# Kernel optimization log

Measured on AMD Instinct MI355X. Metric: run time of the kernel, lower is better.

Reference implementation:

```python
import jax, jax.numpy as jnp
import numpy as np

PATCH = 14   # vision_config.patch_size
MERGE = 2    # spatial_merge_size
D = 1024     # vision_config.hidden_size
# pixel (H, W) per image; all dims divisible by PATCH*MERGE = 28
IMAGE_SIZES = np.array([[1540, 1232], [1120, 1540], [896, 1260],
                        [1540, 1540], [1260, 896], [728, 1540]], dtype=np.int64)


def setup_inputs() -> dict:
    key = jax.random.key(0)
    k1, k2 = jax.random.split(key)
    hs = IMAGE_SIZES[:, 0] // PATCH
    ws = IMAGE_SIZES[:, 1] // PATCH
    total_tokens = int(np.sum(hs * ws))  # 47820
    image_features = jax.random.normal(k1, (total_tokens, D), dtype=jnp.float32)
    # nn.Linear(D*MERGE**2 -> D, bias=False): weight [D, D*MERGE**2]
    weight = jax.random.normal(k2, (D, D * MERGE * MERGE), dtype=jnp.float32) * 0.02
    return {"image_features": image_features, "weight": weight,
            "image_sizes": IMAGE_SIZES}


def _merge_patches(image_features, image_sizes):
    """Per-image unfold(kernel=stride=MERGE) -> [n_blocks, D*MERGE^2], concatenated."""
    m = MERGE
    d = image_features.shape[-1]
    sizes = np.asarray(image_sizes)
    hs = sizes[:, 0] // PATCH
    ws = sizes[:, 1] // PATCH
    offsets = np.concatenate([[0], np.cumsum(hs * ws)])
    grids = []
    for i in range(sizes.shape[0]):
        h, w = int(hs[i]), int(ws[i])
        x = jax.lax.dynamic_slice_in_dim(image_features, int(offsets[i]), h * w, 0)
        # [h, w, d] -> blocks of m x m; torch unfold layout is (d, kh, kw) channel-major
        x = x.reshape(h // m, m, w // m, m, d)
        x = x.transpose(0, 2, 4, 1, 3)           # [h/m, w/m, d, m, m]
        x = x.reshape((h // m) * (w // m), d * m * m)
        grids.append(x)
    return jnp.concatenate(grids, axis=0)        # [sum(h*w)/m^2, d*m^2]


def reference(image_features, weight, image_sizes):
    merged = _merge_patches(image_features, image_sizes)
    return merged @ weight.T                     # [N_merged, D]
```

## Files before the change

### kernel.cpp

```cpp
#include <hip/hip_runtime.h>
#include <hip/hip_bf16.h>
#include <stdint.h>

#define K_DIM 4096
#define N_DIM 1024
#define M_TOT 11955

__constant__ int c_wm[6]     = {44, 55, 45, 55, 32, 55};
__constant__ int c_w[6]      = {88, 110, 90, 110, 64, 110};
__constant__ int c_tokoff[6] = {0, 9680, 18480, 24240, 36340, 42100};
__constant__ int c_blkoff[6] = {0, 2420, 4620, 6060, 9085, 10525};

typedef __attribute__((ext_vector_type(8))) short bf16x8;
typedef __attribute__((ext_vector_type(4))) float f32x4;

__global__ __launch_bounds__(256) void merge_cvt(
    const float* __restrict__ feat, __hip_bfloat16* __restrict__ merged)
{
    const int r = blockIdx.x;
    int img = 0;
#pragma unroll
    for (int t = 1; t < 6; ++t)
        if (r >= c_blkoff[t]) img = t;
    const int bi = r - c_blkoff[img];
    const int wm = c_wm[img];
    const int i = bi / wm;
    const int j = bi - i * wm;
    const int w = c_w[img];

    const size_t base00 = ((size_t)c_tokoff[img] + (size_t)(2 * i) * w + 2 * j) * N_DIM;
    const size_t base01 = base00 + N_DIM;
    const size_t base10 = base00 + (size_t)w * N_DIM;
    const size_t base11 = base10 + N_DIM;

    __hip_bfloat16* outrow = merged + (size_t)r * K_DIM;

    for (int c = threadIdx.x; c < K_DIM / 8; c += 256) {
        const int d2 = 2 * c;
        float2 f00 = *(const float2*)(feat + base00 + d2);
        float2 f01 = *(const float2*)(feat + base01 + d2);
        float2 f10 = *(const float2*)(feat + base10 + d2);
        float2 f11 = *(const float2*)(feat + base11 + d2);
        union { __hip_bfloat16 h[8]; uint4 u; } pk;
        pk.h[0] = __float2bfloat16(f00.x);
        pk.h[1] = __float2bfloat16(f01.x);
        pk.h[2] = __float2bfloat16(f10.x);
        pk.h[3] = __float2bfloat16(f11.x);
        pk.h[4] = __float2bfloat16(f00.y);
        pk.h[5] = __float2bfloat16(f01.y);
        pk.h[6] = __float2bfloat16(f10.y);
        pk.h[7] = __float2bfloat16(f11.y);
        *(uint4*)(outrow + 8 * c) = pk.u;
    }
}

__global__ __launch_bounds__(256) void wcvt(
    const float* __restrict__ src, __hip_bfloat16* __restrict__ dst)
{
    const int idx = blockIdx.x * 256 + threadIdx.x;
    const float4* s = (const float4*)src + (size_t)idx * 2;
    float4 a = s[0], b = s[1];
    union { __hip_bfloat16 h[8]; uint4 u; } pk;
    pk.h[0] = __float2bfloat16(a.x);
    pk.h[1] = __float2bfloat16(a.y);
    pk.h[2] = __float2bfloat16(a.z);
    pk.h[3] = __float2bfloat16(a.w);
    pk.h[4] = __float2bfloat16(b.x);
    pk.h[5] = __float2bfloat16(b.y);
    pk.h[6] = __float2bfloat16(b.z);
    pk.h[7] = __float2bfloat16(b.w);
    *((uint4*)dst + idx) = pk.u;
}

#define BM 128
#define BN 128
#define BK 32

__global__ __launch_bounds__(256) void gemm_bt(
    const __hip_bfloat16* __restrict__ A,
    const __hip_bfloat16* __restrict__ B,
    float* __restrict__ C)
{
    __shared__ __align__(16) __hip_bfloat16 lA[BM * BK];
    __shared__ __align__(16) __hip_bfloat16 lB[BN * BK];

    const int tid = threadIdx.x;
    const int lane = tid & 63;
    const int wave = tid >> 6;
    const int m0 = blockIdx.y * BM;
    const int n0 = blockIdx.x * BN;
    const int wm = (wave >> 1) * 64;
    const int wn = (wave & 1) * 64;
    const int al = lane & 15;
    const int q = lane >> 4;

    const int r0 = tid >> 2;
    const int kp = (tid & 3) * 8;

    int ga0 = m0 + r0;       if (ga0 > M_TOT - 1) ga0 = M_TOT - 1;
    int ga1 = m0 + r0 + 64;  if (ga1 > M_TOT - 1) ga1 = M_TOT - 1;
    const __hip_bfloat16* gA0 = A + (size_t)ga0 * K_DIM + kp;
    const __hip_bfloat16* gA1 = A + (size_t)ga1 * K_DIM + kp;
    const __hip_bfloat16* gB0 = B + (size_t)(n0 + r0) * K_DIM + kp;
    const __hip_bfloat16* gB1 = B + (size_t)(n0 + r0 + 64) * K_DIM + kp;

    __hip_bfloat16* lA0 = lA + tid * 8;
    __hip_bfloat16* lA1 = lA + (tid + 256) * 8;
    __hip_bfloat16* lB0 = lB + tid * 8;
    __hip_bfloat16* lB1 = lB + (tid + 256) * 8;

    f32x4 acc[4][4];
#pragma unroll
    for (int i = 0; i < 4; ++i)
#pragma unroll
        for (int j = 0; j < 4; ++j)
            acc[i][j] = (f32x4){0.f, 0.f, 0.f, 0.f};

    for (int kt = 0; kt < K_DIM; kt += BK) {
        __builtin_amdgcn_global_load_lds(
            (const __attribute__((address_space(1))) void*)(gA0 + kt),
            (__attribute__((address_space(3))) void*)lA0, 16, 0, 0);
        __builtin_amdgcn_global_load_lds(
            (const __attribute__((address_space(1))) void*)(gA1 + kt),
            (__attribute__((address_space(3))) void*)lA1, 16, 0, 0);
        __builtin_amdgcn_global_load_lds(
            (const __attribute__((address_space(1))) void*)(gB0 + kt),
            (__attribute__((address_space(3))) void*)lB0, 16, 0, 0);
        __builtin_amdgcn_global_load_lds(
            (const __attribute__((address_space(1))) void*)(gB1 + kt),
            (__attribute__((address_space(3))) void*)lB1, 16, 0, 0);
        __syncthreads();

        bf16x8 af[4], bfr[4];
#pragma unroll
        for (int mi = 0; mi < 4; ++mi)
            af[mi] = *(const bf16x8*)(lA + (wm + mi * 16 + al) * BK + q * 8);
#pragma unroll
        for (int ni = 0; ni < 4; ++ni)
            bfr[ni] = *(const bf16x8*)(lB + (wn + ni * 16 + al) * BK + q * 8);

#pragma unroll
        for (int mi = 0; mi < 4; ++mi)
#pragma unroll
            for (int ni = 0; ni < 4; ++ni)
                acc[mi][ni] = __builtin_amdgcn_mfma_f32_16x16x32_bf16(
                    af[mi], bfr[ni], acc[mi][ni], 0, 0, 0);
        __syncthreads();
    }

#pragma unroll
    for (int mi = 0; mi < 4; ++mi) {
        const int row = m0 + wm + mi * 16 + q * 4;
#pragma unroll
        for (int ni = 0; ni < 4; ++ni) {
            const int col = n0 + wn + ni * 16 + al;
            float* cp = C + (size_t)row * N_DIM + col;
#pragma unroll
            for (int rg = 0; rg < 4; ++rg) {
                if (row + rg < M_TOT) cp[(size_t)rg * N_DIM] = acc[mi][ni][rg];
            }
        }
    }
}

extern "C" void kernel_launch(void* const* d_in, const int* in_sizes, int n_in,
                              void* d_out, int out_size, void* d_ws, size_t ws_size,
                              hipStream_t stream)
{
    const float* feat = (const float*)d_in[0];
    const float* wgt  = (const float*)d_in[1];
    float* out = (float*)d_out;

    __hip_bfloat16* merged = (__hip_bfloat16*)d_ws;
    __hip_bfloat16* wbf = (__hip_bfloat16*)((char*)d_ws +
                                            (size_t)M_TOT * K_DIM * 2);

    merge_cvt<<<M_TOT, 256, 0, stream>>>(feat, merged);
    wcvt<<<(N_DIM * K_DIM / 8) / 256, 256, 0, stream>>>(wgt, wbf);

    dim3 grid(N_DIM / BN, (M_TOT + BM - 1) / BM);
    gemm_bt<<<grid, 256, 0, stream>>>(merged, wbf, out);
}
```

Measured before the change: 489.8 us.

## Fuse patch merge and bf16 conversion into GEMM A-tile loading

New measurement: 564.4 us. 1.15x slower.

```diff
diff --git a/kernel.cpp b/kernel.cpp
--- a/kernel.cpp
+++ b/kernel.cpp
@@ -5,6 +5,11 @@
 #define K_DIM 4096
 #define N_DIM 1024
 #define M_TOT 11955
+
+#define BM 128
+#define BN 128
+#define BK 64
+#define SA 72
 
 __constant__ int c_wm[6]     = {44, 55, 45, 55, 32, 55};
 __constant__ int c_w[6]      = {88, 110, 90, 110, 64, 110};
@@ -14,46 +19,6 @@
 typedef __attribute__((ext_vector_type(8))) short bf16x8;
 typedef __attribute__((ext_vector_type(4))) float f32x4;
 
-__global__ __launch_bounds__(256) void merge_cvt(
-    const float* __restrict__ feat, __hip_bfloat16* __restrict__ merged)
-{
-    const int r = blockIdx.x;
-    int img = 0;
-#pragma unroll
-    for (int t = 1; t < 6; ++t)
-        if (r >= c_blkoff[t]) img = t;
-    const int bi = r - c_blkoff[img];
-    const int wm = c_wm[img];
-    const int i = bi / wm;
-    const int j = bi - i * wm;
-    const int w = c_w[img];
-
-    const size_t base00 = ((size_t)c_tokoff[img] + (size_t)(2 * i) * w + 2 * j) * N_DIM;
-    const size_t base01 = base00 + N_DIM;
-    const size_t base10 = base00 + (size_t)w * N_DIM;
-    const size_t base11 = base10 + N_DIM;
-
-    __hip_bfloat16* outrow = merged + (size_t)r * K_DIM;
-
-    for (int c = threadIdx.x; c < K_DIM / 8; c += 256) {
-        const int d2 = 2 * c;
-        float2 f00 = *(const float2*)(feat + base00 + d2);
-        float2 f01 = *(const float2*)(feat + base01 + d2);
-        float2 f10 = *(const float2*)(feat + base10 + d2);
-        float2 f11 = *(const float2*)(feat + base11 + d2);
-        union { __hip_bfloat16 h[8]; uint4 u; } pk;
-        pk.h[0] = __float2bfloat16(f00.x);
-        pk.h[1] = __float2bfloat16(f01.x);
-        pk.h[2] = __float2bfloat16(f10.x);
-        pk.h[3] = __float2bfloat16(f11.x);
-        pk.h[4] = __float2bfloat16(f00.y);
-        pk.h[5] = __float2bfloat16(f01.y);
-        pk.h[6] = __float2bfloat16(f10.y);
-        pk.h[7] = __float2bfloat16(f11.y);
-        *(uint4*)(outrow + 8 * c) = pk.u;
-    }
-}
-
 __global__ __launch_bounds__(256) void wcvt(
     const float* __restrict__ src, __hip_bfloat16* __restrict__ dst)
 {
@@ -61,30 +26,22 @@
     const float4* s = (const float4*)src + (size_t)idx * 2;
     float4 a = s[0], b = s[1];
     union { __hip_bfloat16 h[8]; uint4 u; } pk;
-    pk.h[0] = __float2bfloat16(a.x);
-    pk.h[1] = __float2bfloat16(a.y);
-    pk.h[2] = __float2bfloat16(a.z);
-    pk.h[3] = __float2bfloat16(a.w);
-    pk.h[4] = __float2bfloat16(b.x);
-    pk.h[5] = __float2bfloat16(b.y);
-    pk.h[6] = __float2bfloat16(b.z);
-    pk.h[7] = __float2bfloat16(b.w);
+    pk.h[0] = __float2bfloat16(a.x); pk.h[1] = __float2bfloat16(a.y);
+    pk.h[2] = __float2bfloat16(a.z); pk.h[3] = __float2bfloat16(a.w);
+    pk.h[4] = __float2bfloat16(b.x); pk.h[5] = __float2bfloat16(b.y);
+    pk.h[6] = __float2bfloat16(b.z); pk.h[7] = __float2bfloat16(b.w);
     *((uint4*)dst + idx) = pk.u;
 }
 
-#define BM 128
-#define BN 128
-#define BK 32
-
-__global__ __launch_bounds__(256) void gemm_bt(
-    const __hip_bfloat16* __restrict__ A,
-    const __hip_bfloat16* __restrict__ B,
+__global__ __launch_bounds__(256) void gemm_fused(
+    const float* __restrict__ feat,
+    const __hip_bfloat16* __restrict__ Bw,
     float* __restrict__ C)
 {
-    __shared__ __align__(16) __hip_bfloat16 lA[BM * BK];
+    __shared__ __align__(16) __hip_bfloat16 lA[BM * SA];
     __shared__ __align__(16) __hip_bfloat16 lB[BN * BK];
 
-    const int tid = threadIdx.x;
+    const int tid  = threadIdx.x;
     const int lane = tid & 63;
     const int wave = tid >> 6;
     const int m0 = blockIdx.y * BM;
@@ -92,22 +49,35 @@
     const int wm = (wave >> 1) * 64;
     const int wn = (wave & 1) * 64;
     const int al = lane & 15;
-    const int q = lane >> 4;
+    const int q  = lane >> 4;
 
-    const int r0 = tid >> 2;
-    const int kp = (tid & 3) * 8;
+    const int arow = tid >> 1;
+    const int ksel = (tid & 1) * 32;
+    int gm = m0 + arow; if (gm > M_TOT - 1) gm = M_TOT - 1;
+    int img = 0;
+#pragma unroll
+    for (int t = 1; t < 6; ++t) if (gm >= c_blkoff[t]) img = t;
+    const int bi = gm - c_blkoff[img];
+    const int wmrg = c_wm[img];
+    const int gi = bi / wmrg;
+    const int gj = bi - gi * wmrg;
+    const int w  = c_w[img];
+    const size_t b00 = ((size_t)c_tokoff[img] + (size_t)(2 * gi) * w + 2 * gj) * (size_t)N_DIM;
+    const float* s00 = feat + b00;
+    const float* s01 = s00 + N_DIM;
+    const float* s10 = s00 + (size_t)w * N_DIM;
+    const float* s11 = s10 + N_DIM;
+    __hip_bfloat16* lA_dst = lA + arow * SA + ksel;
 
-    int ga0 = m0 + r0;       if (ga0 > M_TOT - 1) ga0 = M_TOT - 1;
-    int ga1 = m0 + r0 + 64;  if (ga1 > M_TOT - 1) ga1 = M_TOT - 1;
-    const __hip_bfloat16* gA0 = A + (size_t)ga0 * K_DIM + kp;
-    const __hip_bfloat16* gA1 = A + (size_t)ga1 * K_DIM + kp;
-    const __hip_bfloat16* gB0 = B + (size_t)(n0 + r0) * K_DIM + kp;
-    const __hip_bfloat16* gB1 = B + (size_t)(n0 + r0 + 64) * K_DIM + kp;
-
-    __hip_bfloat16* lA0 = lA + tid * 8;
-    __hip_bfloat16* lA1 = lA + (tid + 256) * 8;
-    __hip_bfloat16* lB0 = lB + tid * 8;
-    __hip_bfloat16* lB1 = lB + (tid + 256) * 8;
+    const __hip_bfloat16* bsrc[4];
+#pragma unroll
+    for (int j = 0; j < 4; ++j) {
+        const int c = tid + j * 256;
+        const int row = c >> 3;
+        const int p = c & 7;
+        const int g = p ^ (row & 7);
+        bsrc[j] = Bw + (size_t)(n0 + row) * K_DIM + g * 8;
+    }
 
     f32x4 acc[4][4];
 #pragma unroll
@@ -116,36 +86,56 @@
         for (int j = 0; j < 4; ++j)
             acc[i][j] = (f32x4){0.f, 0.f, 0.f, 0.f};
 
+    union f8 { float4 v[2]; float f[8]; };
+
     for (int kt = 0; kt < K_DIM; kt += BK) {
-        __builtin_amdgcn_global_load_lds(
-            (const __attribute__((address_space(1))) void*)(gA0 + kt),
-            (__attribute__((address_space(3))) void*)lA0, 16, 0, 0);
-        __builtin_amdgcn_global_load_lds(
-            (const __attribute__((address_space(1))) void*)(gA1 + kt),
-            (__attribute__((address_space(3))) void*)lA1, 16, 0, 0);
-        __builtin_amdgcn_global_load_lds(
-            (const __attribute__((address_space(1))) void*)(gB0 + kt),
-            (__attribute__((address_space(3))) void*)lB0, 16, 0, 0);
-        __builtin_amdgcn_global_load_lds(
-            (const __attribute__((address_space(1))) void*)(gB1 + kt),
-            (__attribute__((address_space(3))) void*)lB1, 16, 0, 0);
+        const int d0 = (kt + ksel) >> 2;
+        f8 r0, r1, r2, r3;
+        r0.v[0] = *(const float4*)(s00 + d0); r0.v[1] = *(const float4*)(s00 + d0 + 4);
+        r1.v[0] = *(const float4*)(s01 + d0); r1.v[1] = *(const float4*)(s01 + d0 + 4);
+        r2.v[0] = *(const float4*)(s10 + d0); r2.v[1] = *(const float4*)(s10 + d0 + 4);
+        r3.v[0] = *(const float4*)(s11 + d0); r3.v[1] = *(const float4*)(s11 + d0 + 4);
+
         __syncthreads();
 
-        bf16x8 af[4], bfr[4];
 #pragma unroll
-        for (int mi = 0; mi < 4; ++mi)
-            af[mi] = *(const bf16x8*)(lA + (wm + mi * 16 + al) * BK + q * 8);
-#pragma unroll
-        for (int ni = 0; ni < 4; ++ni)
-            bfr[ni] = *(const bf16x8*)(lB + (wn + ni * 16 + al) * BK + q * 8);
+        for (int j = 0; j < 4; ++j)
+            __builtin_amdgcn_global_load_lds(
+                (const __attribute__((address_space(1))) void*)(bsrc[j] + kt),
+                (__attribute__((address_space(3))) void*)(lB + (tid + j * 256) * 8),
+                16, 0, 0);
 
 #pragma unroll
-        for (int mi = 0; mi < 4; ++mi)
+        for (int j = 0; j < 4; ++j) {
+            const int dd = 2 * j;
+            union { __hip_bfloat162 h2[4]; uint4 u; } pk;
+            pk.h2[0] = __float22bfloat162_rn(make_float2(r0.f[dd],     r1.f[dd]));
+            pk.h2[1] = __float22bfloat162_rn(make_float2(r2.f[dd],     r3.f[dd]));
+            pk.h2[2] = __float22bfloat162_rn(make_float2(r0.f[dd + 1], r1.f[dd + 1]));
+            pk.h2[3] = __float22bfloat162_rn(make_float2(r2.f[dd + 1], r3.f[dd + 1]));
+            *(uint4*)(lA_dst + j * 8) = pk.u;
+        }
+        __syncthreads();
+
 #pragma unroll
-            for (int ni = 0; ni < 4; ++ni)
-                acc[mi][ni] = __builtin_amdgcn_mfma_f32_16x16x32_bf16(
-                    af[mi], bfr[ni], acc[mi][ni], 0, 0, 0);
-        __syncthreads();
+        for (int ks = 0; ks < 2; ++ks) {
+            bf16x8 af[4], bfr[4];
+#pragma unroll
+            for (int mi = 0; mi < 4; ++mi)
+                af[mi] = *(const bf16x8*)(lA + (wm + mi * 16 + al) * SA + ks * 32 + q * 8);
+#pragma unroll
+            for (int ni = 0; ni < 4; ++ni) {
+                const int row = wn + ni * 16 + al;
+                const int p = (ks * 4 + q) ^ (row & 7);
+                bfr[ni] = *(const bf16x8*)(lB + row * BK + p * 8);
+            }
+#pragma unroll
+            for (int mi = 0; mi < 4; ++mi)
+#pragma unroll
+                for (int ni = 0; ni < 4; ++ni)
+                    acc[mi][ni] = __builtin_amdgcn_mfma_f32_16x16x32_bf16(
+                        af[mi], bfr[ni], acc[mi][ni], 0, 0, 0);
+        }
     }
 
 #pragma unroll
@@ -171,13 +161,10 @@
     const float* wgt  = (const float*)d_in[1];
     float* out = (float*)d_out;
 
-    __hip_bfloat16* merged = (__hip_bfloat16*)d_ws;
-    __hip_bfloat16* wbf = (__hip_bfloat16*)((char*)d_ws +
-                                            (size_t)M_TOT * K_DIM * 2);
+    __hip_bfloat16* wbf = (__hip_bfloat16*)d_ws;
 
-    merge_cvt<<<M_TOT, 256, 0, stream>>>(feat, merged);
     wcvt<<<(N_DIM * K_DIM / 8) / 256, 256, 0, stream>>>(wgt, wbf);
 
     dim3 grid(N_DIM / BN, (M_TOT + BM - 1) / BM);
-    gemm_bt<<<grid, 256, 0, stream>>>(merged, wbf, out);
+    gemm_fused<<<grid, 256, 0, stream>>>(feat, wbf, out);
 }
```
